# Kernel optimization log

Measured on AMD Instinct MI355X. Metric: run time of the kernel, lower is better.

Reference implementation:

```python
import jax, jax.numpy as jnp
import numpy as np

B, N, P, K, D = 8, 2048, 64, 32, 384
DEPTH, DI, DS, DCONV, DTR, NC = 12, 768, 16, 4, 24, 40
BN_EPS = 1e-5


def _spread_bits(v):
    v = v & 1023
    v = (v | (v << 16)) & 50331903
    v = (v | (v << 8)) & 50393103
    v = (v | (v << 4)) & 51130563
    v = (v | (v << 2)) & 153391689
    return v


def _zkey(x, y, z):
    return _spread_bits(x) | (_spread_bits(y) << 1) | (_spread_bits(z) << 2)


def _sfc_order(xyz, trans):
    lo = xyz.min(0, keepdims=True)
    hi = xyz.max(0, keepdims=True)
    q = jnp.clip(((xyz - lo) / (hi - lo + 1e-6) * 1023.0).astype(jnp.int32), 0, 1023)
    if trans:
        keys = _zkey(q[:, 2], q[:, 1], q[:, 0])
    else:
        keys = _zkey(q[:, 0], q[:, 1], q[:, 2])
    return jnp.argsort(keys)


def _ln(x, g, b):
    m = x.mean(-1, keepdims=True)
    v = jnp.var(x, axis=-1, keepdims=True)
    return (x - m) / jnp.sqrt(v + 1e-5) * g + b


def _bn_eval(x, g, b):
    # BatchNorm in eval mode, running_mean=0 / running_var=1
    return x * (g / np.float32(np.sqrt(1.0 + BN_EPS))) + b


def _patch_embed_one(xyz, w1, b1, g1, be1, w2, b2, g2, be2, w3, b3, g3, be3):
    # xyz: (N,3)
    cidx = (jnp.arange(P) * (N / P)).astype(jnp.int32)
    centers = xyz[cidx]                                      # (P,3)
    d2 = ((centers[:, None, :] - xyz[None, :, :]) ** 2).sum(-1)  # (P,N)
    _, knn = jax.lax.top_k(-d2, K)                           # (P,K) smallest dists
    nx = xyz[knn] - centers[:, None, :]                      # (P,K,3)
    h = jax.nn.gelu(_bn_eval(nx @ w1.T + b1, g1, be1), approximate=False)   # (P,K,64)
    h = jax.nn.gelu(_bn_eval(h @ w2.T + b2, g2, be2), approximate=False)    # (P,K,128)
    h = _bn_eval(h @ w3.T + b3, g3, be3)                     # (P,K,384)
    return h.max(1), centers


def _mamba(x, in_w, conv_w, conv_b, xp_w, dt_w, dt_b, Alog, Dp, out_w):
    # x: (B,L,D)
    Bsz, L, _ = x.shape
    xz = x @ in_w.T                                          # (B,L,2*DI)
    xc, z = xz[..., :DI], xz[..., DI:]
    xpad = jnp.pad(xc, ((0, 0), (DCONV - 1, 0), (0, 0)))
    xc = sum(xpad[:, j:j + L, :] * conv_w[:, j] for j in range(DCONV)) + conv_b
    xc = jax.nn.silu(xc)
    x_dbl = xc @ xp_w.T                                      # (B,L,DTR+2*DS)
    dt = x_dbl[..., :DTR]
    Bm = x_dbl[..., DTR:DTR + DS]
    Cm = x_dbl[..., DTR + DS:]
    delta = jax.nn.softplus(dt @ dt_w.T + dt_b)              # (B,L,DI)
    A = -jnp.exp(Alog)                                       # (DI,DS)

    def step(h, inp):
        d_t, B_t, C_t, u_t = inp                             # (B,DI),(B,DS),(B,DS),(B,DI)
        h = h * jnp.exp(d_t[..., None] * A) + (d_t * u_t)[..., None] * B_t[:, None, :]
        return h, jnp.einsum('bds,bs->bd', h, C_t)

    h0 = jnp.zeros((Bsz, DI, DS), x.dtype)
    inps = (delta.transpose(1, 0, 2), Bm.transpose(1, 0, 2),
            Cm.transpose(1, 0, 2), xc.transpose(1, 0, 2))
    _, ys = jax.lax.scan(step, h0, inps)                     # (L,B,DI)
    y = ys.transpose(1, 0, 2) + Dp * xc
    y = y * jax.nn.silu(z)
    return y @ out_w.T


def setup_inputs() -> dict:
    key = jax.random.key(0)
    ks = iter(jax.random.split(key, 64))
    nrm = lambda *s: jax.random.normal(next(ks), s, jnp.float32) * 0.02
    inp = {
        'data': jax.random.normal(next(ks), (B, N, 3), jnp.float32),
        'pe_w1': nrm(64, 3), 'pe_b1': jnp.zeros(64), 'pe_g1': jnp.ones(64), 'pe_be1': jnp.zeros(64),
        'pe_w2': nrm(128, 64), 'pe_b2': jnp.zeros(128), 'pe_g2': jnp.ones(128), 'pe_be2': jnp.zeros(128),
        'pe_w3': nrm(D, 128), 'pe_b3': jnp.zeros(D), 'pe_g3': jnp.ones(D), 'pe_be3': jnp.zeros(D),
        'oi_h_scale': jnp.ones(D), 'oi_h_shift': jnp.zeros(D),
        'oi_th_scale': jnp.ones(D), 'oi_th_shift': jnp.zeros(D),
        'pos_embed': nrm(1, P, D),
        'blk_ln_g': jnp.ones((DEPTH, D)), 'blk_ln_b': jnp.zeros((DEPTH, D)),
        'blk_in_w': nrm(DEPTH, 2 * DI, D),
        'blk_conv_w': nrm(DEPTH, DI, DCONV), 'blk_conv_b': jnp.zeros((DEPTH, DI)),
        'blk_xp_w': nrm(DEPTH, DTR + 2 * DS, DI),
        'blk_dt_w': nrm(DEPTH, DI, DTR), 'blk_dt_b': jnp.full((DEPTH, DI), -4.0),
        'blk_Alog': jnp.tile(jnp.log(jnp.arange(1, DS + 1, dtype=jnp.float32)), (DEPTH, DI, 1)),
        'blk_D': jnp.ones((DEPTH, DI)),
        'blk_out_w': nrm(DEPTH, D, DI),
        'norm_g': jnp.ones(D), 'norm_b': jnp.zeros(D),
        'mlp_w1': nrm(256, D), 'mlp_b1': jnp.zeros(256),
        'mlp_w2': nrm(64, 256), 'mlp_b2': jnp.zeros(64),
        'mlp_w3': nrm(NC, 64), 'mlp_b3': jnp.zeros(NC),
    }
    return inp


def reference(data, pe_w1, pe_b1, pe_g1, pe_be1, pe_w2, pe_b2, pe_g2, pe_be2,
              pe_w3, pe_b3, pe_g3, pe_be3, oi_h_scale, oi_h_shift, oi_th_scale,
              oi_th_shift, pos_embed, blk_ln_g, blk_ln_b, blk_in_w, blk_conv_w,
              blk_conv_b, blk_xp_w, blk_dt_w, blk_dt_b, blk_Alog, blk_D,
              blk_out_w, norm_g, norm_b, mlp_w1, mlp_b1, mlp_w2, mlp_b2,
              mlp_w3, mlp_b3):
    xyz = data[:, :, :3]
    tokens, centers = jax.vmap(
        _patch_embed_one, in_axes=(0,) + (None,) * 12)(
        xyz, pe_w1, pe_b1, pe_g1, pe_be1, pe_w2, pe_b2, pe_g2, pe_be2,
        pe_w3, pe_b3, pe_g3, pe_be3)                         # (B,P,D),(B,P,3)
    order_h = jax.vmap(lambda c: _sfc_order(c, False))(centers)
    order_th = jax.vmap(lambda c: _sfc_order(c, True))(centers)
    th = jnp.take_along_axis(tokens, order_h[:, :, None], axis=1) * oi_h_scale + oi_h_shift
    tth = jnp.take_along_axis(tokens, order_th[:, :, None], axis=1) * oi_th_scale + oi_th_shift
    t = jnp.concatenate([th + pos_embed, tth + pos_embed], axis=1)  # (B,2P,D)
    for i in range(DEPTH):
        t = t + _mamba(_ln(t, blk_ln_g[i], blk_ln_b[i]),
                       blk_in_w[i], blk_conv_w[i], blk_conv_b[i], blk_xp_w[i],
                       blk_dt_w[i], blk_dt_b[i], blk_Alog[i], blk_D[i], blk_out_w[i])
    t = _ln(t, norm_g, norm_b)
    x = t.mean(1)
    x = jax.nn.relu(x @ mlp_w1.T + mlp_b1)
    x = jax.nn.relu(x @ mlp_w2.T + mlp_b2)
    return x @ mlp_w3.T + mlp_b3
```

## Files before the change

### kernel.cpp

```cpp
#include <hip/hip_runtime.h>
#include <math.h>

#define BB 8
#define NN 2048
#define PP 64
#define KK 32
#define DD 384
#define DEPTH 12
#define DI 768
#define DS 16
#define DCONV 4
#define DTR 24
#define NC 40
#define LL 128
#define XROW (DTR + 2 * DS)
#define NR (BB * LL)

using bf16x8 = __attribute__((ext_vector_type(8))) short;
using floatx4 = __attribute__((ext_vector_type(4))) float;

__device__ __forceinline__ float gelu_exact(float x) {
    return 0.5f * x * (1.0f + erff(x * 0.70710678118654752440f));
}
__device__ __forceinline__ float siluf(float x) {
    return x / (1.0f + expf(-x));
}
__device__ __forceinline__ unsigned short f2bf(float f) {
    unsigned u = __float_as_uint(f);
    u += 0x7fffu + ((u >> 16) & 1u);
    return (unsigned short)(u >> 16);
}
__device__ __forceinline__ float bf2f(short s) {
    return __uint_as_float(((unsigned)(unsigned short)s) << 16);
}
__device__ __forceinline__ unsigned spread_bits(unsigned v) {
    v &= 1023u;
    v = (v | (v << 16)) & 50331903u;
    v = (v | (v << 8)) & 50393103u;
    v = (v | (v << 4)) & 51130563u;
    v = (v | (v << 2)) & 153391689u;
    return v;
}

__global__ void k_cvt(const float* __restrict__ in_w, const float* __restrict__ out_w,
                      const float* __restrict__ pe_w3, const float* __restrict__ xp,
                      unsigned short* __restrict__ inwbf, unsigned short* __restrict__ owbf,
                      unsigned short* __restrict__ w3bf, unsigned short* __restrict__ xpbf)
{
    int idx = (blockIdx.x * 256 + threadIdx.x) * 4;
    const int n1 = DEPTH * 2 * DI * DD;
    const int n2 = DEPTH * DD * DI;
    const int n3 = DD * 128;
    const int n4 = DEPTH * 64 * DI;
    if (idx < n1) {
        float4 v = *(const float4*)(in_w + idx);
        ushort4 o; o.x = f2bf(v.x); o.y = f2bf(v.y); o.z = f2bf(v.z); o.w = f2bf(v.w);
        *(ushort4*)(inwbf + idx) = o;
        return;
    }
    idx -= n1;
    if (idx < n2) {
        float4 v = *(const float4*)(out_w + idx);
        ushort4 o; o.x = f2bf(v.x); o.y = f2bf(v.y); o.z = f2bf(v.z); o.w = f2bf(v.w);
        *(ushort4*)(owbf + idx) = o;
        return;
    }
    idx -= n2;
    if (idx < n3) {
        float4 v = *(const float4*)(pe_w3 + idx);
        ushort4 o; o.x = f2bf(v.x); o.y = f2bf(v.y); o.z = f2bf(v.z); o.w = f2bf(v.w);
        *(ushort4*)(w3bf + idx) = o;
        return;
    }
    idx -= n3;
    if (idx < n4) {
        int i = idx / (64 * DI);
        int rem = idx - i * 64 * DI;
        int n = rem / DI, k = rem % DI;
        ushort4 o;
        if (n < XROW) {
            float4 v = *(const float4*)(xp + (size_t)i * XROW * DI + (size_t)n * DI + k);
            o.x = f2bf(v.x); o.y = f2bf(v.y); o.z = f2bf(v.z); o.w = f2bf(v.w);
        } else {
            o.x = o.y = o.z = o.w = 0;
        }
        *(ushort4*)(xpbf + (size_t)i * 64 * DI + (size_t)n * DI + k) = o;
    }
}

__global__ __launch_bounds__(256) void k_patch(
    const float* __restrict__ data,
    const float* __restrict__ w1, const float* __restrict__ b1,
    const float* __restrict__ g1, const float* __restrict__ be1,
    const float* __restrict__ w2, const float* __restrict__ b2,
    const float* __restrict__ g2, const float* __restrict__ be2,
    const unsigned short* __restrict__ w3bf, const float* __restrict__ b3,
    const float* __restrict__ g3, const float* __restrict__ be3,
    float* __restrict__ tokens, float* __restrict__ centers)
{
    const int bp = blockIdx.x;
    const int b = bp >> 6, p = bp & 63;
    const int tid = threadIdx.x;
    const float* X = data + (size_t)b * NN * 3;
    const float inv_den = 0.99999500003749968752f;

    __shared__ int hist[256];
    __shared__ int klist[KK];
    __shared__ int eqlist[256];
    __shared__ int s_kth, s_byte, s_cnt, s_eqcnt;
    __shared__ float nxs[KK * 3];
    __shared__ float h1s[KK * 64];
    __shared__ short h2b[KK * 136];

    const float cx = X[p * 32 * 3 + 0];
    const float cy = X[p * 32 * 3 + 1];
    const float cz = X[p * 32 * 3 + 2];
    if (tid == 0) {
        centers[(b * PP + p) * 3 + 0] = cx;
        centers[(b * PP + p) * 3 + 1] = cy;
        centers[(b * PP + p) * 3 + 2] = cz;
        s_kth = KK; s_cnt = 0; s_eqcnt = 0;
    }

    {
        const int lane = tid & 63, wid = tid >> 6;
        unsigned key[8];
#pragma unroll
        for (int q = 0; q < 8; q++) {
            int i = tid + 256 * q;
            float dx = cx - X[i * 3 + 0];
            float dy = cy - X[i * 3 + 1];
            float dz = cz - X[i * 3 + 2];
            float d2 = dx * dx + dy * dy + dz * dz;
            key[q] = __float_as_uint(d2);
        }
        unsigned prefix = 0;
        for (int rnd = 3; rnd >= 0; rnd--) {
            const int sh = rnd * 8;
            const unsigned pmask = (rnd == 3) ? 0u : (0xFFFFFFFFu << (8 * (rnd + 1)));
            hist[tid] = 0;
            __syncthreads();
#pragma unroll
            for (int q = 0; q < 8; q++)
                if ((key[q] & pmask) == prefix)
                    atomicAdd(&hist[(key[q] >> sh) & 255], 1);
            __syncthreads();
            if (wid == 0) {
                int c[4], tot = 0;
#pragma unroll
                for (int j = 0; j < 4; j++) { c[j] = hist[lane * 4 + j]; tot += c[j]; }
                int inc = tot;
#pragma unroll
                for (int off = 1; off < 64; off <<= 1) {
                    int u = __shfl_up(inc, off);
                    if (lane >= off) inc += u;
                }
                int exc = inc - tot;
                int kth = s_kth;
                bool has = (exc < kth) && (exc + tot >= kth);
                unsigned long long bal = __ballot(has);
                int src = __ffsll(bal) - 1;
                if (lane == src) {
                    int rem = kth - exc;
                    int j = 0, cum = 0;
                    while (cum + c[j] < rem) { cum += c[j]; j++; }
                    s_byte = lane * 4 + j;
                    s_kth = rem - cum;
                }
            }
            __syncthreads();
            prefix |= ((unsigned)s_byte) << sh;
        }
        const unsigned kstar = prefix;
        const int need = s_kth;
#pragma unroll
        for (int q = 0; q < 8; q++) {
            int i = tid + 256 * q;
            if (key[q] < kstar) {
                int pos = atomicAdd(&s_cnt, 1);
                klist[pos] = i;
            } else if (key[q] == kstar) {
                int pos = atomicAdd(&s_eqcnt, 1);
                if (pos < 256) eqlist[pos] = i;
            }
        }
        __syncthreads();
        if (tid == 0) {
            int base = s_cnt;
            int ne = s_eqcnt < 256 ? s_eqcnt : 256;
            for (int k = 0; k < need; k++) {
                int best = 0x7fffffff, bi = 0;
                for (int j = 0; j < ne; j++)
                    if (eqlist[j] < best) { best = eqlist[j]; bi = j; }
                klist[base + k] = best;
                eqlist[bi] = 0x7fffffff;
            }
        }
        __syncthreads();
    }

    if (tid < KK) {
        int q = klist[tid];
        nxs[tid * 3 + 0] = X[q * 3 + 0] - cx;
        nxs[tid * 3 + 1] = X[q * 3 + 1] - cy;
        nxs[tid * 3 + 2] = X[q * 3 + 2] - cz;
    }
    __syncthreads();

    for (int e = tid; e < KK * 64; e += 256) {
        int j = e >> 6, c = e & 63;
        float v = nxs[j * 3 + 0] * w1[c * 3 + 0] + nxs[j * 3 + 1] * w1[c * 3 + 1] +
                  nxs[j * 3 + 2] * w1[c * 3 + 2] + b1[c];
        v = v * (g1[c] * inv_den) + be1[c];
        h1s[j * 64 + c] = gelu_exact(v);
    }
    __syncthreads();

    for (int e = tid; e < KK * 128; e += 256) {
        int j = e >> 7, c = e & 127;
        const float4* wr = (const float4*)(w2 + (size_t)c * 64);
        const float4* hr = (const float4*)(h1s + j * 64);
        float acc = 0.f;
#pragma unroll
        for (int q = 0; q < 16; q++) {
            float4 wv = wr[q], hv = hr[q];
            acc += hv.x * wv.x + hv.y * wv.y + hv.z * wv.z + hv.w * wv.w;
        }
        float v = (acc + b2[c]) * (g2[c] * inv_den) + be2[c];
        h2b[j * 136 + c] = (short)f2bf(gelu_exact(v));
    }
    __syncthreads();

    const int wave = tid >> 6, lane = tid & 63;
    const int quad = lane >> 4, r = lane & 15;
    floatx4 acc3[2][6] = {};
#pragma unroll
    for (int ks = 0; ks < 4; ks++) {
        const int k0 = ks * 32;
        bf16x8 af[2];
        af[0] = *(const bf16x8*)(h2b + (size_t)r * 136 + quad * 8 + k0);
        af[1] = *(const bf16x8*)(h2b + (size_t)(16 + r) * 136 + quad * 8 + k0);
        bf16x8 bfv[6];
#pragma unroll
        for (int nj = 0; nj < 6; nj++) {
            int n = wave * 96 + nj * 16 + r;
            bfv[nj] = *(const bf16x8*)(w3bf + (size_t)n * 128 + quad * 8 + k0);
        }
#pragma unroll
        for (int mi = 0; mi < 2; mi++)
#pragma unroll
            for (int nj = 0; nj < 6; nj++)
                acc3[mi][nj] = __builtin_amdgcn_mfma_f32_16x16x32_bf16(af[mi], bfv[nj], acc3[mi][nj], 0, 0, 0);
    }
#pragma unroll
    for (int nj = 0; nj < 6; nj++) {
        int col = wave * 96 + nj * 16 + r;
        float sc = g3[col] * inv_den;
        float offc = b3[col] * sc + be3[col];
        float m = -3.4e38f;
#pragma unroll
        for (int mi = 0; mi < 2; mi++)
#pragma unroll
            for (int r2 = 0; r2 < 4; r2++)
                m = fmaxf(m, acc3[mi][nj][r2] * sc + offc);
        m = fmaxf(m, __shfl_xor(m, 16));
        m = fmaxf(m, __shfl_xor(m, 32));
        if (quad == 0) tokens[(size_t)bp * DD + col] = m;
    }
}

__global__ __launch_bounds__(256) void k_sfc_build(
    const float* __restrict__ centers, const float* __restrict__ tokens,
    const float* __restrict__ hs, const float* __restrict__ hb,
    const float* __restrict__ ts2, const float* __restrict__ tb2,
    const float* __restrict__ pos, float* __restrict__ tout)
{
    const int b = blockIdx.y, part = blockIdx.x;
    const int tid = threadIdx.x;

    __shared__ float csh[PP][3];
    __shared__ float slo[3], shi[3];
    __shared__ unsigned khs[PP], kts[PP];
    __shared__ int oh[PP], ot[PP];

    if (tid < PP) {
        csh[tid][0] = centers[(b * PP + tid) * 3 + 0];
        csh[tid][1] = centers[(b * PP + tid) * 3 + 1];
        csh[tid][2] = centers[(b * PP + tid) * 3 + 2];
    }
    __syncthreads();
    if (tid == 0) {
        for (int k = 0; k < 3; k++) {
            float lo = csh[0][k], hi = csh[0][k];
            for (int j = 1; j < PP; j++) { lo = fminf(lo, csh[j][k]); hi = fmaxf(hi, csh[j][k]); }
            slo[k] = lo; shi[k] = hi;
        }
    }
    __syncthreads();
    if (tid < PP) {
        int q[3];
        for (int k = 0; k < 3; k++) {
            float t = (csh[tid][k] - slo[k]) / (shi[k] - slo[k] + 1e-6f) * 1023.0f;
            int qi = (int)t;
            qi = qi < 0 ? 0 : (qi > 1023 ? 1023 : qi);
            q[k] = qi;
        }
        khs[tid] = spread_bits((unsigned)q[0]) | (spread_bits((unsigned)q[1]) << 1) |
                   (spread_bits((unsigned)q[2]) << 2);
        kts[tid] = spread_bits((unsigned)q[2]) | (spread_bits((unsigned)q[1]) << 1) |
                   (spread_bits((unsigned)q[0]) << 2);
    }
    __syncthreads();
    if (tid < PP) {
        unsigned kh = khs[tid], kt = kts[tid];
        int rh = 0, rt = 0;
        for (int j = 0; j < PP; j++) {
            unsigned a = khs[j];
            rh += (a < kh) || (a == kh && j < tid);
            unsigned c = kts[j];
            rt += (c < kt) || (c == kt && j < tid);
        }
        oh[rh] = tid;
        ot[rt] = tid;
    }
    __syncthreads();

    const int base = part * (LL * DD / 24);
    for (int e = tid; e < LL * DD / 24; e += 256) {
        int idx = base + e;
        int d = idx % DD;
        int l = idx / DD;
        float v;
        if (l < PP) {
            int src = oh[l];
            v = tokens[((size_t)b * PP + src) * DD + d] * hs[d] + hb[d] + pos[l * DD + d];
        } else {
            int l2 = l - PP;
            int src = ot[l2];
            v = tokens[((size_t)b * PP + src) * DD + d] * ts2[d] + tb2[d] + pos[l2 * DD + d];
        }
        tout[(size_t)b * LL * DD + idx] = v;
    }
}

__global__ __launch_bounds__(256) void k_stats(const float* __restrict__ t,
                                               const float* __restrict__ g,
                                               const float* __restrict__ gb,
                                               unsigned short* __restrict__ tbf,
                                               float* __restrict__ xdbl)
{
    const int tid = threadIdx.x;
    {
        int gi = blockIdx.x * 256 + tid;
        if (gi < NR * XROW) xdbl[gi] = 0.f;
    }
    const int wid = tid >> 6, lane = tid & 63;
    const int row = blockIdx.x * 4 + wid;
    const size_t base = (size_t)row * DD;
    float v[6];
    float s = 0.f, q = 0.f;
#pragma unroll
    for (int j = 0; j < 6; j++) {
        v[j] = t[base + lane + 64 * j];
        s += v[j]; q += v[j] * v[j];
    }
#pragma unroll
    for (int off = 32; off; off >>= 1) { s += __shfl_xor(s, off); q += __shfl_xor(q, off); }
    float mean = s * (1.0f / DD);
    float var = q * (1.0f / DD) - mean * mean;
    float inv = 1.0f / sqrtf(var + 1e-5f);
#pragma unroll
    for (int j = 0; j < 6; j++) {
        int i = lane + 64 * j;
        tbf[base + i] = f2bf((v[j] - mean) * inv * g[i] + gb[i]);
    }
}

__global__ __launch_bounds__(256) void k_mfma_xz(
    const unsigned short* __restrict__ tbf,
    const unsigned short* __restrict__ inwbf,
    const float* __restrict__ cw, const float* __restrict__ cb,
    const unsigned short* __restrict__ xpbf,
    unsigned short* __restrict__ xcbf, unsigned short* __restrict__ zsbf,
    float* __restrict__ xdbl)
{
    __shared__ short ct[128][72];
    const int tid = threadIdx.x;
    const int wave = tid >> 6, lane = tid & 63;
    const int quad = lane >> 4, r = lane & 15;
    const int wm = wave >> 1, wn = wave & 1;
    const int b = blockIdx.y;
    const int n0 = blockIdx.x * 64;
    const int m0 = b * 128 + wm * 64;

    floatx4 acc[4][2] = {};
    const unsigned short* Ab = tbf + (size_t)(m0 + r) * DD + quad * 8;
    const unsigned short* Bb = inwbf + (size_t)(n0 + wn * 32 + r) * DD + quad * 8;
    for (int k0 = 0; k0 < DD; k0 += 32) {
        bf16x8 af[4], bfv[2];
#pragma unroll
        for (int i = 0; i < 4; i++)
            af[i] = *(const bf16x8*)(Ab + (size_t)(i * 16) * DD + k0);
#pragma unroll
        for (int j = 0; j < 2; j++)
            bfv[j] = *(const bf16x8*)(Bb + (size_t)(j * 16) * DD + k0);
#pragma unroll
        for (int i = 0; i < 4; i++)
#pragma unroll
            for (int j = 0; j < 2; j++)
                acc[i][j] = __builtin_amdgcn_mfma_f32_16x16x32_bf16(af[i], bfv[j], acc[i][j], 0, 0, 0);
    }

#pragma unroll
    for (int i = 0; i < 4; i++)
#pragma unroll
        for (int r2 = 0; r2 < 4; r2++) {
            short* cp = &ct[wm * 64 + i * 16 + quad * 4 + r2][wn * 32 + r];
#pragma unroll
            for (int j = 0; j < 2; j++)
                cp[j * 16] = (short)f2bf(acc[i][j][r2]);
        }
    __syncthreads();

    const int l0 = (tid >> 3) * 4;
    const int c0 = (tid & 7) * 8;
    if (n0 < DI) {
        float cwv[8][4], cbv[8];
#pragma unroll
        for (int q = 0; q < 8; q++) {
            *(float4*)cwv[q] = *(const float4*)(cw + (size_t)(n0 + c0 + q) * 4);
            cbv[q] = cb[n0 + c0 + q];
        }
        unsigned short ov[4][8];
#pragma unroll
        for (int dl = 0; dl < 4; dl++) {
            const int l = l0 + dl;
            float u[8];
#pragma unroll
            for (int q = 0; q < 8; q++) u[q] = cbv[q];
#pragma unroll
            for (int j = 0; j < DCONV; j++) {
                int lt = l - (DCONV - 1) + j;
                if (lt >= 0) {
                    bf16x8 x = *(const bf16x8*)&ct[lt][c0];
#pragma unroll
                    for (int q = 0; q < 8; q++) u[q] += bf2f(x[q]) * cwv[q][j];
                }
            }
#pragma unroll
            for (int q = 0; q < 8; q++) ov[dl][q] = f2bf(siluf(u[q]));
        }
        __syncthreads();
#pragma unroll
        for (int dl = 0; dl < 4; dl++) {
            const int l = l0 + dl;
            *(bf16x8*)&ct[l][c0] = *(bf16x8*)ov[dl];
            *(bf16x8*)(xcbf + (size_t)(b * LL + l) * DI + n0 + c0) = *(bf16x8*)ov[dl];
        }
        __syncthreads();

        floatx4 acc2[2][4] = {};
#pragma unroll
        for (int k0 = 0; k0 < 64; k0 += 32) {
            bf16x8 af2[2], bfv2[4];
#pragma unroll
            for (int i = 0; i < 2; i++)
                af2[i] = *(const bf16x8*)&ct[wave * 32 + i * 16 + r][k0 + quad * 8];
#pragma unroll
            for (int nj = 0; nj < 4; nj++)
                bfv2[nj] = *(const bf16x8*)(xpbf + (size_t)(nj * 16 + r) * DI + n0 + k0 + quad * 8);
#pragma unroll
            for (int i = 0; i < 2; i++)
#pragma unroll
                for (int nj = 0; nj < 4; nj++)
                    acc2[i][nj] = __builtin_amdgcn_mfma_f32_16x16x32_bf16(af2[i], bfv2[nj], acc2[i][nj], 0, 0, 0);
        }
#pragma unroll
        for (int i = 0; i < 2; i++)
#pragma unroll
            for (int nj = 0; nj < 4; nj++) {
                int col = nj * 16 + r;
                if (col < XROW) {
#pragma unroll
                    for (int r2 = 0; r2 < 4; r2++) {
                        int row = b * LL + wave * 32 + i * 16 + quad * 4 + r2;
                        unsafeAtomicAdd(&xdbl[(size_t)row * XROW + col], acc2[i][nj][r2]);
                    }
                }
            }
    } else {
        const int nz = n0 - DI;
#pragma unroll
        for (int dl = 0; dl < 4; dl++) {
            const int l = l0 + dl;
            bf16x8 x = *(const bf16x8*)&ct[l][c0];
            unsigned short o[8];
#pragma unroll
            for (int q = 0; q < 8; q++) o[q] = f2bf(siluf(bf2f(x[q])));
            *(bf16x8*)(zsbf + (size_t)(b * LL + l) * DI + nz + c0) = *(bf16x8*)o;
        }
    }
}

__global__ __launch_bounds__(128) void k_scan(
    const float* __restrict__ xdbl,
    const unsigned short* __restrict__ xcbf, const unsigned short* __restrict__ zsbf,
    const float* __restrict__ dtw, const float* __restrict__ dtb,
    const float* __restrict__ Alog, const float* __restrict__ Dp,
    unsigned short* __restrict__ ybf)
{
    const int tid = threadIdx.x;
    const int b = blockIdx.x / DI;
    const int d = blockIdx.x % DI;

    __shared__ float sdel[LL];
    __shared__ float sdus[LL];
    __shared__ float sus[LL];
    __shared__ float szs[LL];
    __shared__ float negA[DS];
    __shared__ float ApL[DS][9];
    __shared__ float HlL[DS][9];
    __shared__ float hst[DS][9];

    {
        const int t = tid;
        const size_t row = (size_t)b * LL + t;
        const float* xd = xdbl + row * XROW;
        const float* w = dtw + d * DTR;
        float acc = dtb[d];
#pragma unroll
        for (int k = 0; k < DTR; k += 4) {
            float4 xv = *(const float4*)(xd + k);
            float4 wv = *(const float4*)(w + k);
            acc += xv.x * wv.x + xv.y * wv.y + xv.z * wv.z + xv.w * wv.w;
        }
        float delta = fmaxf(acc, 0.f) + log1pf(__expf(-fabsf(acc)));
        float u = bf2f((short)xcbf[row * DI + d]);
        sdel[t] = delta;
        sdus[t] = delta * u;
        sus[t] = u;
        szs[t] = bf2f((short)zsbf[row * DI + d]);
    }
    if (tid < DS) negA[tid] = -__expf(Alog[d * DS + tid]);
    __syncthreads();

    const int s = tid & 15;
    const int c = tid >> 4;
    const float* xB = xdbl + ((size_t)b * LL + c * 16) * XROW + DTR + s;

    float a_r[16], duB_r[16], C_r[16];
    {
        float h = 0.f, Ap = 1.f;
        const float na = negA[s];
#pragma unroll
        for (int q = 0; q < 16; q++) {
            int t = c * 16 + q;
            float a = __expf(sdel[t] * na);
            float Bv = xB[(size_t)q * XROW];
            float Cv = xB[(size_t)q * XROW + DS];
            a_r[q] = a;
            duB_r[q] = sdus[t] * Bv;
            C_r[q] = Cv;
            h = h * a + duB_r[q];
            Ap *= a;
        }
        ApL[s][c] = Ap;
// ... 141 lines not shown
        for (int k = 0; k < 64; k++) acc += h2[k] * wr[k];
        out[b * NC + tid] = acc;
    }
}

extern "C" void kernel_launch(void* const* d_in, const int* in_sizes, int n_in,
                              void* d_out, int out_size, void* d_ws, size_t ws_size,
                              hipStream_t stream)
{
    const float* data      = (const float*)d_in[0];
    const float* pe_w1     = (const float*)d_in[1];
    const float* pe_b1     = (const float*)d_in[2];
    const float* pe_g1     = (const float*)d_in[3];
    const float* pe_be1    = (const float*)d_in[4];
    const float* pe_w2     = (const float*)d_in[5];
    const float* pe_b2     = (const float*)d_in[6];
    const float* pe_g2     = (const float*)d_in[7];
    const float* pe_be2    = (const float*)d_in[8];
    const float* pe_w3     = (const float*)d_in[9];
    const float* pe_b3     = (const float*)d_in[10];
    const float* pe_g3     = (const float*)d_in[11];
    const float* pe_be3    = (const float*)d_in[12];
    const float* oi_h_scale  = (const float*)d_in[13];
    const float* oi_h_shift  = (const float*)d_in[14];
    const float* oi_th_scale = (const float*)d_in[15];
    const float* oi_th_shift = (const float*)d_in[16];
    const float* pos_embed = (const float*)d_in[17];
    const float* blk_ln_g  = (const float*)d_in[18];
    const float* blk_ln_b  = (const float*)d_in[19];
    const float* blk_in_w  = (const float*)d_in[20];
    const float* blk_conv_w = (const float*)d_in[21];
    const float* blk_conv_b = (const float*)d_in[22];
    const float* blk_xp_w  = (const float*)d_in[23];
    const float* blk_dt_w  = (const float*)d_in[24];
    const float* blk_dt_b  = (const float*)d_in[25];
    const float* blk_Alog  = (const float*)d_in[26];
    const float* blk_D     = (const float*)d_in[27];
    const float* blk_out_w = (const float*)d_in[28];
    const float* norm_g    = (const float*)d_in[29];
    const float* norm_b    = (const float*)d_in[30];
    const float* mlp_w1    = (const float*)d_in[31];
    const float* mlp_b1    = (const float*)d_in[32];
    const float* mlp_w2    = (const float*)d_in[33];
    const float* mlp_b2    = (const float*)d_in[34];
    const float* mlp_w3    = (const float*)d_in[35];
    const float* mlp_b3    = (const float*)d_in[36];

    float* ws = (float*)d_ws;
    size_t off = 0;
    auto alloc = [&](size_t n) { float* p = ws + off; off += (n + 63) & ~(size_t)63; return p; };
    float* tokens  = alloc((size_t)BB * PP * DD);
    float* centers = alloc((size_t)BB * PP * 3);
    float* t    = alloc((size_t)NR * DD);
    float* xdbl = alloc((size_t)NR * XROW);
    float* pparts  = alloc((size_t)BB * 8 * DD);
    unsigned short* tbf   = (unsigned short*)alloc((size_t)NR * DD / 2);
    unsigned short* xcbf  = (unsigned short*)alloc((size_t)NR * DI / 2);
    unsigned short* zsbf  = (unsigned short*)alloc((size_t)NR * DI / 2);
    unsigned short* ybf   = (unsigned short*)alloc((size_t)NR * DI / 2);
    unsigned short* inwbf = (unsigned short*)alloc((size_t)DEPTH * 2 * DI * DD / 2);
    unsigned short* owbf  = (unsigned short*)alloc((size_t)DEPTH * DD * DI / 2);
    unsigned short* xpbf  = (unsigned short*)alloc((size_t)DEPTH * 64 * DI / 2);
    unsigned short* w3bf  = (unsigned short*)alloc((size_t)DD * 128 / 2);

    {
        const int total = DEPTH * 2 * DI * DD + DEPTH * DD * DI + DD * 128 + DEPTH * 64 * DI;
        k_cvt<<<(total / 4 + 255) / 256, 256, 0, stream>>>(
            blk_in_w, blk_out_w, pe_w3, blk_xp_w, inwbf, owbf, w3bf, xpbf);
    }

    k_patch<<<BB * PP, 256, 0, stream>>>(data,
        pe_w1, pe_b1, pe_g1, pe_be1, pe_w2, pe_b2, pe_g2, pe_be2,
        w3bf, pe_b3, pe_g3, pe_be3, tokens, centers);
    k_sfc_build<<<dim3(24, BB), 256, 0, stream>>>(centers, tokens,
        oi_h_scale, oi_h_shift, oi_th_scale, oi_th_shift, pos_embed, t);

    for (int i = 0; i < DEPTH; i++) {
        const float* ln_g = blk_ln_g + i * DD;
        const float* ln_b = blk_ln_b + i * DD;
        const float* cw   = blk_conv_w + (size_t)i * DI * DCONV;
        const float* cb   = blk_conv_b + (size_t)i * DI;
        const float* dtw  = blk_dt_w + (size_t)i * DI * DTR;
        const float* dtb  = blk_dt_b + (size_t)i * DI;
        const float* Al   = blk_Alog + (size_t)i * DI * DS;
        const float* Dpp  = blk_D + (size_t)i * DI;
        const unsigned short* inw = inwbf + (size_t)i * 2 * DI * DD;
        const unsigned short* ow  = owbf + (size_t)i * DD * DI;
        const unsigned short* xpb = xpbf + (size_t)i * 64 * DI;

        k_stats<<<NR / 4, 256, 0, stream>>>(t, ln_g, ln_b, tbf, xdbl);
        k_mfma_xz<<<dim3(24, BB), 256, 0, stream>>>(
            tbf, inw, cw, cb, xpb, xcbf, zsbf, xdbl);
        k_scan<<<BB * DI, 128, 0, stream>>>(xdbl, xcbf, zsbf, dtw, dtb, Al, Dpp, ybf);
        k_mfma_op<<<dim3(DD / 64, NR / 32, 2), 256, 0, stream>>>(ybf, ow, t);
    }

    k_lnpool<<<dim3(8, BB), 256, 0, stream>>>(t, norm_g, norm_b, pparts);
    k_mlp<<<BB, 256, 0, stream>>>(pparts, mlp_w1, mlp_b1, mlp_w2, mlp_b2, mlp_w3, mlp_b3,
                                  (float*)d_out);
}
```

Measured before the change: 937.9 us.

## Fuse LayerNorm into in-projection GEMM, double-buffer xdbl zeroing, MFMA patch layer2

Removes the per-layer k_stats kernel by computing LayerNorm statistics and the normalized bf16 A tile inside k_mfma_xz, which now runs 512 threads per block. The xdbl accumulation buffer is double-buffered: the scan kernel zeroes the buffer for the next layer and sfc_build zeroes the first one. In the patch embedding, the second MLP layer moves to bf16 MFMA using a pre-converted w2, and the radix-select histogram is split per wave and per round, which drops one barrier per round. The aim is fewer launches and less global traffic, at the cost of recomputing LN row stats in every column block and more LDS use.

```diff
diff --git a/kernel.cpp b/kernel.cpp
--- a/kernel.cpp
+++ b/kernel.cpp
@@ -44,14 +44,17 @@
 
 __global__ void k_cvt(const float* __restrict__ in_w, const float* __restrict__ out_w,
                       const float* __restrict__ pe_w3, const float* __restrict__ xp,
+                      const float* __restrict__ w2,
                       unsigned short* __restrict__ inwbf, unsigned short* __restrict__ owbf,
-                      unsigned short* __restrict__ w3bf, unsigned short* __restrict__ xpbf)
+                      unsigned short* __restrict__ w3bf, unsigned short* __restrict__ xpbf,
+                      unsigned short* __restrict__ w2bf)
 {
     int idx = (blockIdx.x * 256 + threadIdx.x) * 4;
     const int n1 = DEPTH * 2 * DI * DD;
     const int n2 = DEPTH * DD * DI;
     const int n3 = DD * 128;
     const int n4 = DEPTH * 64 * DI;
+    const int n5 = 128 * 64;
     if (idx < n1) {
         float4 v = *(const float4*)(in_w + idx);
         ushort4 o; o.x = f2bf(v.x); o.y = f2bf(v.y); o.z = f2bf(v.z); o.w = f2bf(v.w);
@@ -85,6 +88,13 @@
             o.x = o.y = o.z = o.w = 0;
         }
         *(ushort4*)(xpbf + (size_t)i * 64 * DI + (size_t)n * DI + k) = o;
+        return;
+    }
+    idx -= n4;
+    if (idx < n5) {
+        float4 v = *(const float4*)(w2 + idx);
+        ushort4 o; o.x = f2bf(v.x); o.y = f2bf(v.y); o.z = f2bf(v.z); o.w = f2bf(v.w);
+        *(ushort4*)(w2bf + idx) = o;
     }
 }
 
@@ -92,7 +102,7 @@
     const float* __restrict__ data,
     const float* __restrict__ w1, const float* __restrict__ b1,
     const float* __restrict__ g1, const float* __restrict__ be1,
-    const float* __restrict__ w2, const float* __restrict__ b2,
+    const unsigned short* __restrict__ w2bf, const float* __restrict__ b2,
     const float* __restrict__ g2, const float* __restrict__ be2,
     const unsigned short* __restrict__ w3bf, const float* __restrict__ b3,
     const float* __restrict__ g3, const float* __restrict__ be3,
@@ -104,13 +114,13 @@
     const float* X = data + (size_t)b * NN * 3;
     const float inv_den = 0.99999500003749968752f;
 
-    __shared__ int hist[256];
+    __shared__ int hist[4][4][256];
     __shared__ int klist[KK];
     __shared__ int eqlist[256];
     __shared__ int s_kth, s_byte, s_cnt, s_eqcnt;
     __shared__ float nxs[KK * 3];
-    __shared__ float h1s[KK * 64];
-    __shared__ short h2b[KK * 136];
+    __shared__ short h1b[KK][72];
+    __shared__ short h2b[KK][136];
 
     const float cx = X[p * 32 * 3 + 0];
     const float cy = X[p * 32 * 3 + 1];
@@ -121,9 +131,11 @@
         centers[(b * PP + p) * 3 + 2] = cz;
         s_kth = KK; s_cnt = 0; s_eqcnt = 0;
     }
+    for (int i = tid; i < 4 * 4 * 256; i += 256) ((int*)hist)[i] = 0;
+
+    const int wave = tid >> 6, lane = tid & 63;
 
     {
-        const int lane = tid & 63, wid = tid >> 6;
         unsigned key[8];
 #pragma unroll
         for (int q = 0; q < 8; q++) {
@@ -134,21 +146,26 @@
             float d2 = dx * dx + dy * dy + dz * dz;
             key[q] = __float_as_uint(d2);
         }
+        __syncthreads();
         unsigned prefix = 0;
         for (int rnd = 3; rnd >= 0; rnd--) {
             const int sh = rnd * 8;
+            const int rslot = 3 - rnd;
             const unsigned pmask = (rnd == 3) ? 0u : (0xFFFFFFFFu << (8 * (rnd + 1)));
-            hist[tid] = 0;
-            __syncthreads();
 #pragma unroll
             for (int q = 0; q < 8; q++)
                 if ((key[q] & pmask) == prefix)
-                    atomicAdd(&hist[(key[q] >> sh) & 255], 1);
+                    atomicAdd(&hist[rslot][wave][(key[q] >> sh) & 255], 1);
             __syncthreads();
-            if (wid == 0) {
+            if (wave == 0) {
                 int c[4], tot = 0;
 #pragma unroll
-                for (int j = 0; j < 4; j++) { c[j] = hist[lane * 4 + j]; tot += c[j]; }
+                for (int j = 0; j < 4; j++) {
+                    int s4 = 0;
+#pragma unroll
+                    for (int w = 0; w < 4; w++) s4 += hist[rslot][w][lane * 4 + j];
+                    c[j] = s4; tot += s4;
+                }
                 int inc = tot;
 #pragma unroll
                 for (int off = 1; off < 64; off <<= 1) {
@@ -212,34 +229,55 @@
         float v = nxs[j * 3 + 0] * w1[c * 3 + 0] + nxs[j * 3 + 1] * w1[c * 3 + 1] +
                   nxs[j * 3 + 2] * w1[c * 3 + 2] + b1[c];
         v = v * (g1[c] * inv_den) + be1[c];
-        h1s[j * 64 + c] = gelu_exact(v);
-    }
-    __syncthreads();
-
-    for (int e = tid; e < KK * 128; e += 256) {
-        int j = e >> 7, c = e & 127;
-        const float4* wr = (const float4*)(w2 + (size_t)c * 64);
-        const float4* hr = (const float4*)(h1s + j * 64);
-        float acc = 0.f;
-#pragma unroll
-        for (int q = 0; q < 16; q++) {
-            float4 wv = wr[q], hv = hr[q];
-            acc += hv.x * wv.x + hv.y * wv.y + hv.z * wv.z + hv.w * wv.w;
-        }
-        float v = (acc + b2[c]) * (g2[c] * inv_den) + be2[c];
-        h2b[j * 136 + c] = (short)f2bf(gelu_exact(v));
-    }
-    __syncthreads();
-
-    const int wave = tid >> 6, lane = tid & 63;
+        h1b[j][c] = (short)f2bf(gelu_exact(v));
+    }
+    __syncthreads();
+
     const int quad = lane >> 4, r = lane & 15;
+
+    {
+        floatx4 acc2[2][2] = {};
+#pragma unroll
+        for (int ks = 0; ks < 2; ks++) {
+            const int k0 = ks * 32;
+            bf16x8 af[2], bfv[2];
+#pragma unroll
+            for (int mi = 0; mi < 2; mi++)
+                af[mi] = *(const bf16x8*)&h1b[mi * 16 + r][quad * 8 + k0];
+#pragma unroll
+            for (int jj = 0; jj < 2; jj++) {
+                int n = wave * 32 + jj * 16 + r;
+                bfv[jj] = *(const bf16x8*)(w2bf + (size_t)n * 64 + quad * 8 + k0);
+            }
+#pragma unroll
+            for (int mi = 0; mi < 2; mi++)
+#pragma unroll
+                for (int jj = 0; jj < 2; jj++)
+                    acc2[mi][jj] = __builtin_amdgcn_mfma_f32_16x16x32_bf16(af[mi], bfv[jj], acc2[mi][jj], 0, 0, 0);
+        }
+#pragma unroll
+        for (int jj = 0; jj < 2; jj++) {
+            int col = wave * 32 + jj * 16 + r;
+            float sc = g2[col] * inv_den;
+            float bb = b2[col] * sc + be2[col];
+#pragma unroll
+            for (int mi = 0; mi < 2; mi++)
+#pragma unroll
+                for (int r2 = 0; r2 < 4; r2++) {
+                    int row = mi * 16 + quad * 4 + r2;
+                    h2b[row][col] = (short)f2bf(gelu_exact(acc2[mi][jj][r2] * sc + bb));
+                }
+        }
+    }
+    __syncthreads();
+
     floatx4 acc3[2][6] = {};
 #pragma unroll
     for (int ks = 0; ks < 4; ks++) {
         const int k0 = ks * 32;
         bf16x8 af[2];
-        af[0] = *(const bf16x8*)(h2b + (size_t)r * 136 + quad * 8 + k0);
-        af[1] = *(const bf16x8*)(h2b + (size_t)(16 + r) * 136 + quad * 8 + k0);
+        af[0] = *(const bf16x8*)&h2b[r][quad * 8 + k0];
+        af[1] = *(const bf16x8*)&h2b[16 + r][quad * 8 + k0];
         bf16x8 bfv[6];
 #pragma unroll
         for (int nj = 0; nj < 6; nj++) {
@@ -273,10 +311,16 @@
     const float* __restrict__ centers, const float* __restrict__ tokens,
     const float* __restrict__ hs, const float* __restrict__ hb,
     const float* __restrict__ ts2, const float* __restrict__ tb2,
-    const float* __restrict__ pos, float* __restrict__ tout)
+    const float* __restrict__ pos, float* __restrict__ tout,
+    float* __restrict__ xd0)
 {
     const int b = blockIdx.y, part = blockIdx.x;
     const int tid = threadIdx.x;
+
+    {
+        int fid = (b * 24 + part) * 256 + tid;
+        for (int i = fid; i < NR * XROW; i += 192 * 256) xd0[i] = 0.f;
+    }
 
     __shared__ float csh[PP][3];
     __shared__ float slo[3], shi[3];
@@ -343,86 +387,97 @@
     }
 }
 
-__global__ __launch_bounds__(256) void k_stats(const float* __restrict__ t,
-                                               const float* __restrict__ g,
-                                               const float* __restrict__ gb,
-                                               unsigned short* __restrict__ tbf,
-                                               float* __restrict__ xdbl)
-{
-    const int tid = threadIdx.x;
-    {
-        int gi = blockIdx.x * 256 + tid;
-        if (gi < NR * XROW) xdbl[gi] = 0.f;
-    }
-    const int wid = tid >> 6, lane = tid & 63;
-    const int row = blockIdx.x * 4 + wid;
-    const size_t base = (size_t)row * DD;
-    float v[6];
-    float s = 0.f, q = 0.f;
-#pragma unroll
-    for (int j = 0; j < 6; j++) {
-        v[j] = t[base + lane + 64 * j];
-        s += v[j]; q += v[j] * v[j];
-    }
-#pragma unroll
-    for (int off = 32; off; off >>= 1) { s += __shfl_xor(s, off); q += __shfl_xor(q, off); }
-    float mean = s * (1.0f / DD);
-    float var = q * (1.0f / DD) - mean * mean;
-    float inv = 1.0f / sqrtf(var + 1e-5f);
-#pragma unroll
-    for (int j = 0; j < 6; j++) {
-        int i = lane + 64 * j;
-        tbf[base + i] = f2bf((v[j] - mean) * inv * g[i] + gb[i]);
-    }
-}
-
-__global__ __launch_bounds__(256) void k_mfma_xz(
-    const unsigned short* __restrict__ tbf,
+__global__ __launch_bounds__(512) void k_mfma_xz(
+    const float* __restrict__ t,
+    const float* __restrict__ ln_g, const float* __restrict__ ln_b,
     const unsigned short* __restrict__ inwbf,
     const float* __restrict__ cw, const float* __restrict__ cb,
     const unsigned short* __restrict__ xpbf,
     unsigned short* __restrict__ xcbf, unsigned short* __restrict__ zsbf,
     float* __restrict__ xdbl)
 {
-    __shared__ short ct[128][72];
+    __shared__ float smean[128], sinv[128];
+    __shared__ short lnA[128][200];
+    short (*ct)[72] = (short (*)[72])&lnA[0][0];
+
     const int tid = threadIdx.x;
     const int wave = tid >> 6, lane = tid & 63;
     const int quad = lane >> 4, r = lane & 15;
     const int wm = wave >> 1, wn = wave & 1;
     const int b = blockIdx.y;
     const int n0 = blockIdx.x * 64;
-    const int m0 = b * 128 + wm * 64;
-
-    floatx4 acc[4][2] = {};
-    const unsigned short* Ab = tbf + (size_t)(m0 + r) * DD + quad * 8;
-    const unsigned short* Bb = inwbf + (size_t)(n0 + wn * 32 + r) * DD + quad * 8;
-    for (int k0 = 0; k0 < DD; k0 += 32) {
-        bf16x8 af[4], bfv[2];
-#pragma unroll
-        for (int i = 0; i < 4; i++)
-            af[i] = *(const bf16x8*)(Ab + (size_t)(i * 16) * DD + k0);
-#pragma unroll
-        for (int j = 0; j < 2; j++)
-            bfv[j] = *(const bf16x8*)(Bb + (size_t)(j * 16) * DD + k0);
-#pragma unroll
-        for (int i = 0; i < 4; i++)
+
+    for (int it = 0; it < 16; it++) {
+        const int row = wave * 16 + it;
+        const float* xr = t + (size_t)(b * LL + row) * DD;
+        float s = 0.f, q = 0.f;
+#pragma unroll
+        for (int j = 0; j < 6; j++) { float v = xr[lane + 64 * j]; s += v; q += v * v; }
+#pragma unroll
+        for (int off = 32; off; off >>= 1) { s += __shfl_xor(s, off); q += __shfl_xor(q, off); }
+        if (lane == 0) {
+            float mean = s * (1.0f / DD);
+            float var = q * (1.0f / DD) - mean * mean;
+            smean[row] = mean;
+            sinv[row] = 1.0f / sqrtf(var + 1e-5f);
+        }
+    }
+    __syncthreads();
+
+    floatx4 acc[2][2] = {};
+    for (int kh = 0; kh < 2; kh++) {
+        {
+            const int row = tid >> 2;
+            const int cb0 = (tid & 3) * 48;
+            const float mean = smean[row];
+            const float inv = sinv[row];
+            const float* xr = t + (size_t)(b * LL + row) * DD + kh * 192 + cb0;
+            const float* gg = ln_g + kh * 192 + cb0;
+            const float* bb = ln_b + kh * 192 + cb0;
+#pragma unroll
+            for (int i = 0; i < 12; i++) {
+                float4 v = *(const float4*)(xr + i * 4);
+                float4 g4 = *(const float4*)(gg + i * 4);
+                float4 b4 = *(const float4*)(bb + i * 4);
+                ushort4 o;
+                o.x = f2bf((v.x - mean) * inv * g4.x + b4.x);
+                o.y = f2bf((v.y - mean) * inv * g4.y + b4.y);
+                o.z = f2bf((v.z - mean) * inv * g4.z + b4.z);
+                o.w = f2bf((v.w - mean) * inv * g4.w + b4.w);
+                *(ushort4*)&lnA[row][cb0 + i * 4] = o;
+            }
+        }
+        __syncthreads();
+        const unsigned short* Bb = inwbf + (size_t)(n0 + wn * 32 + r) * DD + kh * 192 + quad * 8;
+        for (int k0 = 0; k0 < 192; k0 += 32) {
+            bf16x8 af[2], bfv[2];
+#pragma unroll
+            for (int i = 0; i < 2; i++)
+                af[i] = *(const bf16x8*)&lnA[wm * 32 + i * 16 + r][k0 + quad * 8];
 #pragma unroll
             for (int j = 0; j < 2; j++)
-                acc[i][j] = __builtin_amdgcn_mfma_f32_16x16x32_bf16(af[i], bfv[j], acc[i][j], 0, 0, 0);
-    }
-
-#pragma unroll
-    for (int i = 0; i < 4; i++)
+                bfv[j] = *(const bf16x8*)(Bb + (size_t)(j * 16) * DD + k0);
+#pragma unroll
+            for (int i = 0; i < 2; i++)
+#pragma unroll
+                for (int j = 0; j < 2; j++)
+                    acc[i][j] = __builtin_amdgcn_mfma_f32_16x16x32_bf16(af[i], bfv[j], acc[i][j], 0, 0, 0);
+        }
+        __syncthreads();
+    }
+
+#pragma unroll
+    for (int i = 0; i < 2; i++)
 #pragma unroll
         for (int r2 = 0; r2 < 4; r2++) {
-            short* cp = &ct[wm * 64 + i * 16 + quad * 4 + r2][wn * 32 + r];
+            short* cp = &ct[wm * 32 + i * 16 + quad * 4 + r2][wn * 32 + r];
 #pragma unroll
             for (int j = 0; j < 2; j++)
                 cp[j * 16] = (short)f2bf(acc[i][j][r2]);
         }
     __syncthreads();
 
-    const int l0 = (tid >> 3) * 4;
+    const int l0 = (tid >> 3) * 2;
     const int c0 = (tid & 7) * 8;
     if (n0 < DI) {
         float cwv[8][4], cbv[8];
@@ -431,9 +486,9 @@
             *(float4*)cwv[q] = *(const float4*)(cw + (size_t)(n0 + c0 + q) * 4);
             cbv[q] = cb[n0 + c0 + q];
         }
-        unsigned short ov[4][8];
-#pragma unroll
-        for (int dl = 0; dl < 4; dl++) {
+        unsigned short ov[2][8];
+#pragma unroll
+        for (int dl = 0; dl < 2; dl++) {
             const int l = l0 + dl;
             float u[8];
 #pragma unroll
@@ -452,46 +507,40 @@
         }
         __syncthreads();
 #pragma unroll
-        for (int dl = 0; dl < 4; dl++) {
+        for (int dl = 0; dl < 2; dl++) {
             const int l = l0 + dl;
             *(bf16x8*)&ct[l][c0] = *(bf16x8*)ov[dl];
             *(bf16x8*)(xcbf + (size_t)(b * LL + l) * DI + n0 + c0) = *(bf16x8*)ov[dl];
         }
         __syncthreads();
 
-        floatx4 acc2[2][4] = {};
+        floatx4 acc2[4] = {};
 #pragma unroll
         for (int k0 = 0; k0 < 64; k0 += 32) {
-            bf16x8 af2[2], bfv2[4];
-#pragma unroll
-            for (int i = 0; i < 2; i++)
-                af2[i] = *(const bf16x8*)&ct[wave * 32 + i * 16 + r][k0 + quad * 8];
+            bf16x8 af2 = *(const bf16x8*)&ct[wave * 16 + r][k0 + quad * 8];
+            bf16x8 bfv2[4];
 #pragma unroll
             for (int nj = 0; nj < 4; nj++)
                 bfv2[nj] = *(const bf16x8*)(xpbf + (size_t)(nj * 16 + r) * DI + n0 + k0 + quad * 8);
 #pragma unroll
-            for (int i = 0; i < 2; i++)
-#pragma unroll
-                for (int nj = 0; nj < 4; nj++)
-                    acc2[i][nj] = __builtin_amdgcn_mfma_f32_16x16x32_bf16(af2[i], bfv2[nj], acc2[i][nj], 0, 0, 0);
-        }
-#pragma unroll
-        for (int i = 0; i < 2; i++)
-#pragma unroll
-            for (int nj = 0; nj < 4; nj++) {
-                int col = nj * 16 + r;
-                if (col < XROW) {
-#pragma unroll
-                    for (int r2 = 0; r2 < 4; r2++) {
-                        int row = b * LL + wave * 32 + i * 16 + quad * 4 + r2;
-                        unsafeAtomicAdd(&xdbl[(size_t)row * XROW + col], acc2[i][nj][r2]);
-                    }
+            for (int nj = 0; nj < 4; nj++)
+                acc2[nj] = __builtin_amdgcn_mfma_f32_16x16x32_bf16(af2, bfv2[nj], acc2[nj], 0, 0, 0);
+        }
+#pragma unroll
+        for (int nj = 0; nj < 4; nj++) {
+            int col = nj * 16 + r;
+            if (col < XROW) {
+#pragma unroll
+                for (int r2 = 0; r2 < 4; r2++) {
+                    int row = b * LL + wave * 16 + quad * 4 + r2;
+                    unsafeAtomicAdd(&xdbl[(size_t)row * XROW + col], acc2[nj][r2]);
                 }
             }
+        }
     } else {
         const int nz = n0 - DI;
 #pragma unroll
-        for (int dl = 0; dl < 4; dl++) {
+        for (int dl = 0; dl < 2; dl++) {
             const int l = l0 + dl;
             bf16x8 x = *(const bf16x8*)&ct[l][c0];
             unsigned short o[8];
@@ -503,15 +552,18 @@
 }
 
 __global__ __launch_bounds__(128) void k_scan(
-    const float* __restrict__ xdbl,
+    const float* __restrict__ xdbl, float* __restrict__ xdbl_zero,
     const unsigned short* __restrict__ xcbf, const unsigned short* __restrict__ zsbf,
     const float* __restrict__ dtw, const float* __restrict__ dtb,
     const float* __restrict__ Alog, const float* __restrict__ Dp,
     unsigned short* __restrict__ ybf)
 {
     const int tid = threadIdx.x;
-    const int b = blockIdx.x / DI;
-    const int d = blockIdx.x % DI;
+    const int bid = blockIdx.x;
+    const int b = bid / DI;
+    const int d = bid % DI;
+
+    if (bid < (NR * XROW) / 128) xdbl_zero[bid * 128 + tid] = 0.f;
 
     __shared__ float sdel[LL];
     __shared__ float sdus[LL];
@@ -759,9 +811,9 @@
     float* tokens  = alloc((size_t)BB * PP * DD);
     float* centers = alloc((size_t)BB * PP * 3);
     float* t    = alloc((size_t)NR * DD);
-    float* xdbl = alloc((size_t)NR * XROW);
+    float* xd0  = alloc((size_t)NR * XROW);
+    float* xd1  = alloc((size_t)NR * XROW);
     float* pparts  = alloc((size_t)BB * 8 * DD);
-    unsigned short* tbf   = (unsigned short*)alloc((size_t)NR * DD / 2);
     unsigned short* xcbf  = (unsigned short*)alloc((size_t)NR * DI / 2);
     unsigned short* zsbf  = (unsigned short*)alloc((size_t)NR * DI / 2);
     unsigned short* ybf   = (unsigned short*)alloc((size_t)NR * DI / 2);
@@ -769,18 +821,19 @@
     unsigned short* owbf  = (unsigned short*)alloc((size_t)DEPTH * DD * DI / 2);
     unsigned short* xpbf  = (unsigned short*)alloc((size_t)DEPTH * 64 * DI / 2);
     unsigned short* w3bf  = (unsigned short*)alloc((size_t)DD * 128 / 2);
+    unsigned short* w2bf  = (unsigned short*)alloc((size_t)128 * 64 / 2);
 
     {
-        const int total = DEPTH * 2 * DI * DD + DEPTH * DD * DI + DD * 128 + DEPTH * 64 * DI;
+        const int total = DEPTH * 2 * DI * DD + DEPTH * DD * DI + DD * 128 + DEPTH * 64 * DI + 128 * 64;
         k_cvt<<<(total / 4 + 255) / 256, 256, 0, stream>>>(
-            blk_in_w, blk_out_w, pe_w3, blk_xp_w, inwbf, owbf, w3bf, xpbf);
+            blk_in_w, blk_out_w, pe_w3, blk_xp_w, pe_w2, inwbf, owbf, w3bf, xpbf, w2bf);
     }
 
     k_patch<<<BB * PP, 256, 0, stream>>>(data,
-        pe_w1, pe_b1, pe_g1, pe_be1, pe_w2, pe_b2, pe_g2, pe_be2,
+        pe_w1, pe_b1, pe_g1, pe_be1, w2bf, pe_b2, pe_g2, pe_be2,
         w3bf, pe_b3, pe_g3, pe_be3, tokens, centers);
     k_sfc_build<<<dim3(24, BB), 256, 0, stream>>>(centers, tokens,
-        oi_h_scale, oi_h_shift, oi_th_scale, oi_th_shift, pos_embed, t);
+        oi_h_scale, oi_h_shift, oi_th_scale, oi_th_shift, pos_embed, t, xd0);
 
     for (int i = 0; i < DEPTH; i++) {
         const float* ln_g = blk_ln_g + i * DD;
@@ -795,10 +848,12 @@
         const unsigned short* ow  = owbf + (size_t)i * DD * DI;
         const unsigned short* xpb = xpbf + (size_t)i * 64 * DI;
 
-        k_stats<<<NR / 4, 256, 0, stream>>>(t, ln_g, ln_b, tbf, xdbl);
-        k_mfma_xz<<<dim3(24, BB), 256, 0, stream>>>(
-            tbf, inw, cw, cb, xpb, xcbf, zsbf, xdbl);
-        k_scan<<<BB * DI, 128, 0, stream>>>(xdbl, xcbf, zsbf, dtw, dtb, Al, Dpp, ybf);
+        float* xd_rd = (i & 1) ? xd1 : xd0;
+        float* xd_z  = (i & 1) ? xd0 : xd1;
+
+        k_mfma_xz<<<dim3(24, BB), 512, 0, stream>>>(
+            t, ln_g, ln_b, inw, cw, cb, xpb, xcbf, zsbf, xd_rd);
+        k_scan<<<BB * DI, 128, 0, stream>>>(xd_rd, xd_z, xcbf, zsbf, dtw, dtb, Al, Dpp, ybf);
         k_mfma_op<<<dim3(DD / 64, NR / 32, 2), 256, 0, stream>>>(ybf, ow, t);
     }
 
```

Measured after the change: 1.071 ms. 14.2% more time.

## Use MFMA for patch-embed second layer and per-wave radix histograms

Applied to the files above, without the earlier changes.

The second patch-embedding MLP layer (64->128) moves from scalar fp32 dot products to bf16 MFMA, with w2 converted to bf16 in the conversion kernel and h1 stored as bf16 in shared memory. The radix-select kNN histograms are split into per-round, per-wave copies that are zeroed once up front, which cuts atomic contention and the per-round clear-and-sync. This trades extra shared memory and a further bf16 rounding of the layer-2 input and weights for less ALU work and fewer barriers in k_patch.

```diff
diff --git a/kernel.cpp b/kernel.cpp
--- a/kernel.cpp
+++ b/kernel.cpp
@@ -44,14 +44,17 @@
 
 __global__ void k_cvt(const float* __restrict__ in_w, const float* __restrict__ out_w,
                       const float* __restrict__ pe_w3, const float* __restrict__ xp,
+                      const float* __restrict__ w2,
                       unsigned short* __restrict__ inwbf, unsigned short* __restrict__ owbf,
-                      unsigned short* __restrict__ w3bf, unsigned short* __restrict__ xpbf)
+                      unsigned short* __restrict__ w3bf, unsigned short* __restrict__ xpbf,
+                      unsigned short* __restrict__ w2bf)
 {
     int idx = (blockIdx.x * 256 + threadIdx.x) * 4;
     const int n1 = DEPTH * 2 * DI * DD;
     const int n2 = DEPTH * DD * DI;
     const int n3 = DD * 128;
     const int n4 = DEPTH * 64 * DI;
+    const int n5 = 128 * 64;
     if (idx < n1) {
         float4 v = *(const float4*)(in_w + idx);
         ushort4 o; o.x = f2bf(v.x); o.y = f2bf(v.y); o.z = f2bf(v.z); o.w = f2bf(v.w);
@@ -85,6 +88,13 @@
             o.x = o.y = o.z = o.w = 0;
         }
         *(ushort4*)(xpbf + (size_t)i * 64 * DI + (size_t)n * DI + k) = o;
+        return;
+    }
+    idx -= n4;
+    if (idx < n5) {
+        float4 v = *(const float4*)(w2 + idx);
+        ushort4 o; o.x = f2bf(v.x); o.y = f2bf(v.y); o.z = f2bf(v.z); o.w = f2bf(v.w);
+        *(ushort4*)(w2bf + idx) = o;
     }
 }
 
@@ -92,7 +102,7 @@
     const float* __restrict__ data,
     const float* __restrict__ w1, const float* __restrict__ b1,
     const float* __restrict__ g1, const float* __restrict__ be1,
-    const float* __restrict__ w2, const float* __restrict__ b2,
+    const unsigned short* __restrict__ w2bf, const float* __restrict__ b2,
     const float* __restrict__ g2, const float* __restrict__ be2,
     const unsigned short* __restrict__ w3bf, const float* __restrict__ b3,
     const float* __restrict__ g3, const float* __restrict__ be3,
@@ -104,13 +114,13 @@
     const float* X = data + (size_t)b * NN * 3;
     const float inv_den = 0.99999500003749968752f;
 
-    __shared__ int hist[256];
+    __shared__ int hist[4][4][256];
     __shared__ int klist[KK];
     __shared__ int eqlist[256];
     __shared__ int s_kth, s_byte, s_cnt, s_eqcnt;
     __shared__ float nxs[KK * 3];
-    __shared__ float h1s[KK * 64];
-    __shared__ short h2b[KK * 136];
+    __shared__ short h1b[KK][72];
+    __shared__ short h2b[KK][136];
 
     const float cx = X[p * 32 * 3 + 0];
     const float cy = X[p * 32 * 3 + 1];
@@ -121,9 +131,11 @@
         centers[(b * PP + p) * 3 + 2] = cz;
         s_kth = KK; s_cnt = 0; s_eqcnt = 0;
     }
+    for (int i = tid; i < 4 * 4 * 256; i += 256) ((int*)hist)[i] = 0;
+
+    const int wave = tid >> 6, lane = tid & 63;
 
     {
-        const int lane = tid & 63, wid = tid >> 6;
         unsigned key[8];
 #pragma unroll
         for (int q = 0; q < 8; q++) {
@@ -134,21 +146,26 @@
             float d2 = dx * dx + dy * dy + dz * dz;
             key[q] = __float_as_uint(d2);
         }
+        __syncthreads();
         unsigned prefix = 0;
         for (int rnd = 3; rnd >= 0; rnd--) {
             const int sh = rnd * 8;
+            const int rslot = 3 - rnd;
             const unsigned pmask = (rnd == 3) ? 0u : (0xFFFFFFFFu << (8 * (rnd + 1)));
-            hist[tid] = 0;
-            __syncthreads();
 #pragma unroll
             for (int q = 0; q < 8; q++)
                 if ((key[q] & pmask) == prefix)
-                    atomicAdd(&hist[(key[q] >> sh) & 255], 1);
+                    atomicAdd(&hist[rslot][wave][(key[q] >> sh) & 255], 1);
             __syncthreads();
-            if (wid == 0) {
+            if (wave == 0) {
                 int c[4], tot = 0;
 #pragma unroll
-                for (int j = 0; j < 4; j++) { c[j] = hist[lane * 4 + j]; tot += c[j]; }
+                for (int j = 0; j < 4; j++) {
+                    int s4 = 0;
+#pragma unroll
+                    for (int w = 0; w < 4; w++) s4 += hist[rslot][w][lane * 4 + j];
+                    c[j] = s4; tot += s4;
+                }
                 int inc = tot;
 #pragma unroll
                 for (int off = 1; off < 64; off <<= 1) {
@@ -212,34 +229,55 @@
         float v = nxs[j * 3 + 0] * w1[c * 3 + 0] + nxs[j * 3 + 1] * w1[c * 3 + 1] +
                   nxs[j * 3 + 2] * w1[c * 3 + 2] + b1[c];
         v = v * (g1[c] * inv_den) + be1[c];
-        h1s[j * 64 + c] = gelu_exact(v);
-    }
-    __syncthreads();
-
-    for (int e = tid; e < KK * 128; e += 256) {
-        int j = e >> 7, c = e & 127;
-        const float4* wr = (const float4*)(w2 + (size_t)c * 64);
-        const float4* hr = (const float4*)(h1s + j * 64);
-        float acc = 0.f;
-#pragma unroll
-        for (int q = 0; q < 16; q++) {
-            float4 wv = wr[q], hv = hr[q];
-            acc += hv.x * wv.x + hv.y * wv.y + hv.z * wv.z + hv.w * wv.w;
-        }
-        float v = (acc + b2[c]) * (g2[c] * inv_den) + be2[c];
-        h2b[j * 136 + c] = (short)f2bf(gelu_exact(v));
-    }
-    __syncthreads();
-
-    const int wave = tid >> 6, lane = tid & 63;
+        h1b[j][c] = (short)f2bf(gelu_exact(v));
+    }
+    __syncthreads();
+
     const int quad = lane >> 4, r = lane & 15;
+
+    {
+        floatx4 acc2[2][2] = {};
+#pragma unroll
+        for (int ks = 0; ks < 2; ks++) {
+            const int k0 = ks * 32;
+            bf16x8 af[2], bfv[2];
+#pragma unroll
+            for (int mi = 0; mi < 2; mi++)
+                af[mi] = *(const bf16x8*)&h1b[mi * 16 + r][quad * 8 + k0];
+#pragma unroll
+            for (int jj = 0; jj < 2; jj++) {
+                int n = wave * 32 + jj * 16 + r;
+                bfv[jj] = *(const bf16x8*)(w2bf + (size_t)n * 64 + quad * 8 + k0);
+            }
+#pragma unroll
+            for (int mi = 0; mi < 2; mi++)
+#pragma unroll
+                for (int jj = 0; jj < 2; jj++)
+                    acc2[mi][jj] = __builtin_amdgcn_mfma_f32_16x16x32_bf16(af[mi], bfv[jj], acc2[mi][jj], 0, 0, 0);
+        }
+#pragma unroll
+        for (int jj = 0; jj < 2; jj++) {
+            int col = wave * 32 + jj * 16 + r;
+            float sc = g2[col] * inv_den;
+            float bb = b2[col] * sc + be2[col];
+#pragma unroll
+            for (int mi = 0; mi < 2; mi++)
+#pragma unroll
+                for (int r2 = 0; r2 < 4; r2++) {
+                    int row = mi * 16 + quad * 4 + r2;
+                    h2b[row][col] = (short)f2bf(gelu_exact(acc2[mi][jj][r2] * sc + bb));
+                }
+        }
+    }
+    __syncthreads();
+
     floatx4 acc3[2][6] = {};
 #pragma unroll
     for (int ks = 0; ks < 4; ks++) {
         const int k0 = ks * 32;
         bf16x8 af[2];
-        af[0] = *(const bf16x8*)(h2b + (size_t)r * 136 + quad * 8 + k0);
-        af[1] = *(const bf16x8*)(h2b + (size_t)(16 + r) * 136 + quad * 8 + k0);
+        af[0] = *(const bf16x8*)&h2b[r][quad * 8 + k0];
+        af[1] = *(const bf16x8*)&h2b[16 + r][quad * 8 + k0];
         bf16x8 bfv[6];
 #pragma unroll
         for (int nj = 0; nj < 6; nj++) {
@@ -769,15 +807,16 @@
     unsigned short* owbf  = (unsigned short*)alloc((size_t)DEPTH * DD * DI / 2);
     unsigned short* xpbf  = (unsigned short*)alloc((size_t)DEPTH * 64 * DI / 2);
     unsigned short* w3bf  = (unsigned short*)alloc((size_t)DD * 128 / 2);
+    unsigned short* w2bf  = (unsigned short*)alloc((size_t)128 * 64 / 2);
 
     {
-        const int total = DEPTH * 2 * DI * DD + DEPTH * DD * DI + DD * 128 + DEPTH * 64 * DI;
+        const int total = DEPTH * 2 * DI * DD + DEPTH * DD * DI + DD * 128 + DEPTH * 64 * DI + 128 * 64;
         k_cvt<<<(total / 4 + 255) / 256, 256, 0, stream>>>(
-            blk_in_w, blk_out_w, pe_w3, blk_xp_w, inwbf, owbf, w3bf, xpbf);
+            blk_in_w, blk_out_w, pe_w3, blk_xp_w, pe_w2, inwbf, owbf, w3bf, xpbf, w2bf);
     }
 
     k_patch<<<BB * PP, 256, 0, stream>>>(data,
-        pe_w1, pe_b1, pe_g1, pe_be1, pe_w2, pe_b2, pe_g2, pe_be2,
+        pe_w1, pe_b1, pe_g1, pe_be1, w2bf, pe_b2, pe_g2, pe_be2,
         w3bf, pe_b3, pe_g3, pe_be3, tokens, centers);
     k_sfc_build<<<dim3(24, BB), 256, 0, stream>>>(centers, tokens,
         oi_h_scale, oi_h_shift, oi_th_scale, oi_th_shift, pos_embed, t);
```

After: 915.1 us, median of 2. 2.4% less time.
